# Optimization experiments

Hardware: AMD Instinct MI355X
Metric: run time of the kernel (lower is better)

## Reference

```python
import jax, jax.numpy as jnp
import numpy as np

NPOINT = 1024
BRANCHES = [(0.4, 32), (0.8, 64)]  # (radius, nsample)
SPECS = [[67, 64, 64, 128], [67, 64, 128, 256]]  # mlp specs after use_xyz (+3)
EPS = 1e-5


def setup_inputs() -> dict:
    key = jax.random.key(0)
    ks = jax.random.split(key, 16)
    B, N, C = 8, 8192, 64
    inp = {
        "xyz": jax.random.normal(ks[0], (B, N, 3), jnp.float32),
        "features": jax.random.normal(ks[1], (B, C, N), jnp.float32),
    }
    ki = 2
    for bi, spec in enumerate(SPECS):
        for li in range(3):
            o, i = spec[li + 1], spec[li]
            inp[f"w{bi}_{li}"] = jax.random.normal(ks[ki], (o, i), jnp.float32) * (1.0 / np.sqrt(i)); ki += 1
            inp[f"g{bi}_{li}"] = jnp.ones((o,), jnp.float32)
            inp[f"b{bi}_{li}"] = jnp.zeros((o,), jnp.float32)
    return inp


def fps(pts, npoint):
    # pts: [B, N+1, 3] (mean point prepended); sequential farthest point sampling
    B, N1, _ = pts.shape

    def step(carry, _):
        dist, far = carry
        idx3 = jnp.broadcast_to(far[:, None, None], (B, 1, 3))
        centroid = jnp.take_along_axis(pts, idx3, axis=1)  # [B,1,3]
        d = jnp.sum((pts - centroid) ** 2, axis=-1)        # [B,N+1]
        dist = jnp.minimum(dist, d)
        far2 = jnp.argmax(dist, axis=-1)
        return (dist, far2), centroid[:, 0, :]

    dist0 = jnp.full((B, N1), 1e10, jnp.float32)
    far0 = jnp.zeros((B,), jnp.int32)
    _, locs = jax.lax.scan(step, (dist0, far0), None, length=npoint)
    return jnp.transpose(locs, (1, 0, 2))  # [B, npoint, 3]


def ball_query(xyz, new_xyz, radius, nsample):
    # first <=nsample indices with dist^2 < radius^2, padded with first valid (0 if none)
    B, N, _ = xyz.shape
    d2 = jnp.sum((new_xyz[:, :, None, :] - xyz[:, None, :, :]) ** 2, axis=-1)  # [B,S,N]
    score = jnp.where(d2 < radius * radius, jnp.arange(N, dtype=jnp.int32), N)
    vals, _ = jax.lax.top_k(-score, nsample)  # smallest scores = earliest valid indices
    idx = -vals                               # [B,S,nsample], N marks invalid
    first = idx[..., :1]
    first = jnp.where(first < N, first, 0)
    return jnp.where(idx < N, idx, first)


def _forward(xyz, features, params):
    mean = jnp.mean(xyz, axis=1, keepdims=True)
    pts = jnp.concatenate([mean, xyz], axis=1)          # prepend mean point
    new_xyz = jax.lax.stop_gradient(fps(pts, NPOINT))   # [B,npoint,3] (torch no_grad)
    outs = []
    for (radius, nsample), layers in zip(BRANCHES, params):
        idx = ball_query(xyz, new_xyz, radius, nsample)           # [B,S,K]
        gxyz = jax.vmap(lambda p, i: p[i])(xyz, idx)              # [B,S,K,3]
        rel = jnp.transpose(gxyz - new_xyz[:, :, None, :], (0, 3, 1, 2))  # [B,3,S,K]
        gfeat = jax.vmap(lambda f, i: f[:, i])(features, idx)     # [B,C,S,K]
        x = jnp.concatenate([rel, gfeat], axis=1)                 # [B,3+C,S,K]
        for W, g, b in layers:  # Conv2d 1x1 (no bias) + BatchNorm (train stats) + ReLU
            x = jnp.einsum('oi,bisk->bosk', W, x)
            m = jnp.mean(x, axis=(0, 2, 3), keepdims=True)
            v = jnp.var(x, axis=(0, 2, 3), keepdims=True)
            x = (x - m) / jnp.sqrt(v + EPS) * g[None, :, None, None] + b[None, :, None, None]
            x = jax.nn.relu(x)
        outs.append(jnp.max(x, axis=3))                           # [B,Cout,S]
    return new_xyz, jnp.concatenate(outs, axis=1)


def reference(xyz, features,
              w0_0, g0_0, b0_0, w0_1, g0_1, b0_1, w0_2, g0_2, b0_2,
              w1_0, g1_0, b1_0, w1_1, g1_1, b1_1, w1_2, g1_2, b1_2):
    params = [
        [(w0_0, g0_0, b0_0), (w0_1, g0_1, b0_1), (w0_2, g0_2, b0_2)],
        [(w1_0, g1_0, b1_0), (w1_1, g1_1, b1_1), (w1_2, g1_2, b1_2)],
    ]
    return _forward(xyz, features, params)
```

## Files before the change

### kernel.cpp

```cpp
#include <hip/hip_runtime.h>
#include <hip/hip_bf16.h>
#include <cstdint>


typedef __attribute__((ext_vector_type(8))) short short8;
typedef __attribute__((ext_vector_type(4))) float f32x4;
typedef __attribute__((ext_vector_type(2))) float f32x2;

__device__ __forceinline__ float bf2f(unsigned short u) {
    return __uint_as_float(((unsigned)u) << 16);
}
__device__ __forceinline__ unsigned short f2bf(float f) {
    unsigned u = __float_as_uint(f);
    return (unsigned short)((u + 0x7fffu + ((u >> 16) & 1u)) >> 16);
}

__device__ __forceinline__ float wave_red_max_f32(float v) {
#define DPPSTEP(ctrl)                                                                  \
    {                                                                                  \
        int _t = __builtin_amdgcn_update_dpp((int)0xFF800000, __float_as_int(v), ctrl, \
                                             0xf, 0xf, false);                         \
        v = fmaxf(v, __int_as_float(_t));                                              \
    }
    DPPSTEP(0x111) DPPSTEP(0x112) DPPSTEP(0x114) DPPSTEP(0x118) DPPSTEP(0x142) DPPSTEP(0x143)
#undef DPPSTEP
    return v;
}
__device__ __forceinline__ unsigned wave_red_min_u32(unsigned v) {
#define DPPSTEP(ctrl)                                                                   \
    {                                                                                   \
        unsigned _t = (unsigned)__builtin_amdgcn_update_dpp((int)0xFFFFFFFF, (int)v,    \
                                                            ctrl, 0xf, 0xf, false);     \
        v = v < _t ? v : _t;                                                            \
    }
    DPPSTEP(0x111) DPPSTEP(0x112) DPPSTEP(0x114) DPPSTEP(0x118) DPPSTEP(0x142) DPPSTEP(0x143)
#undef DPPSTEP
    return v;
}
__device__ __forceinline__ unsigned long long u64max(unsigned long long a, unsigned long long b) {
    return a > b ? a : b;
}
__device__ __forceinline__ unsigned u32min(unsigned a, unsigned b) { return a < b ? a : b; }

static const size_t OFF_WBF   = 0;
static const size_t OFF_STATS = 262144;
static const size_t STATS_BYTES = 720896;
static const size_t OFF_AFF   = 1048576;
static const size_t OFF_IDX0  = 2097152;
static const size_t OFF_IDX1  = 3145728;
static const size_t OFF_MX    = 5242880;
static const size_t OFF_MN    = 13631488;
static const size_t OFF_Y0    = 22020096;
static const size_t OFF_Y1    = 90177536;
static const size_t OFF_FEATT = 211812352;

__global__ __launch_bounds__(512) void fused_pre(
    const float* __restrict__ xyz, const float* __restrict__ feat,
    float* __restrict__ newxyz, unsigned short* __restrict__ ft,
    const float* __restrict__ w0, const float* __restrict__ w1, const float* __restrict__ w2,
    const float* __restrict__ w3, const float* __restrict__ w4, const float* __restrict__ w5,
    unsigned short* __restrict__ wb) {
    __shared__ union alignas(16) SM {
        struct {
            float ptsx[8200], ptsy[8200], ptsz[8200];
            float ldsM[16][3];
            float meanv[3];
            unsigned long long sKey[2][8];
            float cbuf[3072];
        } f;
        float tile[64][65];
    } sm;
    const int tid = threadIdx.x;

    if (blockIdx.x >= 1032) {
        int id = (int)(blockIdx.x - 1032) * 512 + tid;
        const int psz[6] = {6144, 4096, 8192, 6144, 8192, 32768};
        const int Kp[6] = {96, 64, 64, 96, 64, 128};
        const int Ks[6] = {67, 64, 64, 67, 64, 128};
        const float* wp[6] = {w0, w1, w2, w3, w4, w5};
        int off = 0;
        for (int l = 0; l < 6; ++l) {
            if (id < off + psz[l]) {
                int e = id - off;
                int m = e / Kp[l], k = e - m * Kp[l];
                float v = (k < Ks[l]) ? wp[l][m * Ks[l] + k] : 0.f;
                wb[id] = f2bf(v);
                return;
            }
            off += psz[l];
        }
        return;
    }

    if (blockIdx.x >= 8) {
        int tb = (int)blockIdx.x - 8;
        int b = tb >> 7;
        int j0 = (tb & 127) * 64;
#pragma unroll
        for (int i = 0; i < 8; ++i) {
            int e = i * 512 + tid;
            int c = e >> 6, j = e & 63;
            sm.tile[j][c] = feat[((size_t)b * 64 + c) * 8192 + j0 + j];
        }
        __syncthreads();
#pragma unroll
        for (int i = 0; i < 8; ++i) {
            int e = i * 512 + tid;
            int j = e >> 6, c = e & 63;
            ft[((size_t)(b * 8192 + j0 + j)) * 96 + 3 + c] = f2bf(sm.tile[j][c]);
        }
        if (tid < 64) {
            int j = tid;
            size_t base = ((size_t)(b * 8192 + j0 + j)) * 96;
            const float* xp = xyz + ((size_t)b * 8192 + j0 + j) * 3;
            ft[base + 0] = f2bf(xp[0]);
            ft[base + 1] = f2bf(xp[1]);
            ft[base + 2] = f2bf(xp[2]);
        } else if (tid < 128) {
            int j = tid - 64;
            size_t base = ((size_t)(b * 8192 + j0 + j)) * 96;
            for (int c = 67; c < 96; ++c) ft[base + c] = 0;
        }
        return;
    }

    const int b = blockIdx.x;
    const int t = tid;
    const int lane = t & 63, wv = t >> 6;
    const float* xb = xyz + (size_t)b * 8192 * 3;

    f32x2 px[8], py[8], pz[8], d[8];
#pragma unroll
    for (int k = 0; k < 8; ++k) {
        int q0 = t + 512 * (2 * k);
        int q1 = t + 512 * (2 * k + 1);
        px[k].x = xb[q0 * 3 + 0]; px[k].y = xb[q1 * 3 + 0];
        py[k].x = xb[q0 * 3 + 1]; py[k].y = xb[q1 * 3 + 1];
        pz[k].x = xb[q0 * 3 + 2]; pz[k].y = xb[q1 * 3 + 2];
        d[k].x = 1e10f; d[k].y = 1e10f;
        sm.f.ptsx[q0 + 1] = px[k].x; sm.f.ptsx[q1 + 1] = px[k].y;
        sm.f.ptsy[q0 + 1] = py[k].x; sm.f.ptsy[q1 + 1] = py[k].y;
        sm.f.ptsz[q0 + 1] = pz[k].x; sm.f.ptsz[q1 + 1] = pz[k].y;
    }
    float sxA = 0.f, syA = 0.f, szA = 0.f;
    float sxB = 0.f, syB = 0.f, szB = 0.f;
    int uA = (t + 1023) & 1023;
    int uB = (t + 511) & 1023;
#pragma unroll
    for (int j = 0; j < 8; ++j) {
        int ia = uA + 1024 * j;
        int ib = uB + 1024 * j;
        sxA += xb[ia * 3 + 0]; syA += xb[ia * 3 + 1]; szA += xb[ia * 3 + 2];
        sxB += xb[ib * 3 + 0]; syB += xb[ib * 3 + 1]; szB += xb[ib * 3 + 2];
    }
#pragma unroll
    for (int off = 32; off; off >>= 1) {
        sxA += __shfl_xor(sxA, off, 64);
        syA += __shfl_xor(syA, off, 64);
        szA += __shfl_xor(szA, off, 64);
        sxB += __shfl_xor(sxB, off, 64);
        syB += __shfl_xor(syB, off, 64);
        szB += __shfl_xor(szB, off, 64);
    }
    if (lane == 0) {
        sm.f.ldsM[wv][0] = sxA; sm.f.ldsM[wv][1] = syA; sm.f.ldsM[wv][2] = szA;
        sm.f.ldsM[wv + 8][0] = sxB; sm.f.ldsM[wv + 8][1] = syB; sm.f.ldsM[wv + 8][2] = szB;
    }
    __syncthreads();
    if (t < 3) {
        float s = 0.f;
        for (int w = 0; w < 16; ++w) s += sm.f.ldsM[w][t];
        sm.f.meanv[t] = s * (1.f / 8192.f);
    }
    __syncthreads();
    float cx = sm.f.meanv[0], cy = sm.f.meanv[1], cz = sm.f.meanv[2];
    const float mmx = cx, mmy = cy, mmz = cz;
    float dm = 1e10f;
    if (t == 0) { sm.f.ptsx[0] = cx; sm.f.ptsy[0] = cy; sm.f.ptsz[0] = cz; }
    __syncthreads();

    for (int it = 0; it < 1024; ++it) {
        if (t == 0) {
            sm.f.cbuf[it * 3 + 0] = cx;
            sm.f.cbuf[it * 3 + 1] = cy;
            sm.f.cbuf[it * 3 + 2] = cz;
        }
        f32x2 c0, c1, c2, vm2;
        c0.x = cx; c0.y = cx; c1.x = cy; c1.y = cy; c2.x = cz; c2.y = cz;
        vm2.x = -1e30f; vm2.y = -1e30f;
        {
#pragma clang fp contract(off)
#pragma unroll
            for (int k = 0; k < 8; ++k) {
                f32x2 dx = px[k] - c0;
                f32x2 dy = py[k] - c1;
                f32x2 dz = pz[k] - c2;
                f32x2 dd = (dx * dx + dy * dy) + dz * dz;
                f32x2 nd = __builtin_elementwise_min(d[k], dd);
                d[k] = nd;
                vm2 = __builtin_elementwise_max(vm2, nd);
            }
        }
        float vmax = fmaxf(vm2.x, vm2.y);
        if (t == 0) {
            float dx = __fsub_rn(mmx, cx);
            float dy = __fsub_rn(mmy, cy);
            float dz = __fsub_rn(mmz, cz);
            float dd = __fadd_rn(__fadd_rn(__fmul_rn(dx, dx), __fmul_rn(dy, dy)), __fmul_rn(dz, dz));
            dm = fminf(dm, dd);
            vmax = fmaxf(vmax, dm);
        }
        float wm = wave_red_max_f32(vmax);
        float bmaxw = __int_as_float(__builtin_amdgcn_readlane(__float_as_int(wm), 63));
        unsigned m2[8];
#pragma unroll
        for (int k = 0; k < 8; ++k) {
            unsigned i0 = (d[k].x == bmaxw) ? (unsigned)(t + 512 * (2 * k) + 1) : 0xFFFFFFFFu;
            unsigned i1 = (d[k].y == bmaxw) ? (unsigned)(t + 512 * (2 * k + 1) + 1) : 0xFFFFFFFFu;
            m2[k] = u32min(i0, i1);
        }
        unsigned n0 = u32min(m2[0], m2[1]), n1 = u32min(m2[2], m2[3]);
        unsigned n2 = u32min(m2[4], m2[5]), n3 = u32min(m2[6], m2[7]);
        unsigned mi = u32min(u32min(n0, n1), u32min(n2, n3));
        if (t == 0 && dm == bmaxw) mi = 0u;
        unsigned wmin = wave_red_min_u32(mi);
        unsigned miw = (unsigned)__builtin_amdgcn_readlane((int)wmin, 63);
        int par = it & 1;
        if (lane == 0)
            sm.f.sKey[par][wv] = ((unsigned long long)__float_as_uint(bmaxw) << 32) |
                                 (unsigned long long)(8192u - miw);
        __syncthreads();
        unsigned long long ka[8];
#pragma unroll
        for (int i = 0; i < 8; ++i) ka[i] = sm.f.sKey[par][i];
        unsigned long long p0 = u64max(ka[0], ka[1]), p1 = u64max(ka[2], ka[3]);
        unsigned long long p2 = u64max(ka[4], ka[5]), p3 = u64max(ka[6], ka[7]);
        unsigned long long kk = u64max(u64max(p0, p1), u64max(p2, p3));
        int far = 8192 - (int)(unsigned)(kk & 0xffffffffull);
        cx = sm.f.ptsx[far];
        cy = sm.f.ptsy[far];
        cz = sm.f.ptsz[far];
    }
    __syncthreads();
    float* ob = newxyz + (size_t)b * 3072;
#pragma unroll
    for (int i = 0; i < 6; ++i) ob[t + 512 * i] = sm.f.cbuf[t + 512 * i];
}

__global__ void ball_query_kernel(const float* __restrict__ xyz, const float* __restrict__ newxyz,
                                  int* __restrict__ idxout, float r2, int K) {
    int wid = (blockIdx.x * blockDim.x + threadIdx.x) >> 6;
    int lane = threadIdx.x & 63;
    int b = wid >> 10;
    const float* q = newxyz + (size_t)wid * 3;
    float qx = q[0], qy = q[1], qz = q[2];
    const float* xb = xyz + (size_t)b * 8192 * 3;
    int* out = idxout + (size_t)wid * K;
    int count = 0;
    int first = 0;
    for (int base = 0; base < 8192 && count < K; base += 64) {
        int j = base + lane;
        float dx = __fsub_rn(xb[j * 3 + 0], qx);
        float dy = __fsub_rn(xb[j * 3 + 1], qy);
        float dz = __fsub_rn(xb[j * 3 + 2], qz);
        float d2 = __fadd_rn(__fadd_rn(__fmul_rn(dx, dx), __fmul_rn(dy, dy)), __fmul_rn(dz, dz));
        bool in = d2 < r2;
        unsigned long long m = __ballot(in);
        if (count == 0 && m) first = base + __ffsll((long long)m) - 1;
        if (in) {
            int pos = count + __popcll(m & ((1ull << lane) - 1ull));
            if (pos < K) out[pos] = j;
        }
        count += __popcll(m);
    }
    if (count < K) {
        int fillv = (count > 0) ? first : 0;
        for (int p = count + lane; p < K; p += 64) out[p] = fillv;
    }
}

template <int Mp, int Kp, int IN_MODE, int OUT_MODE, int KSH>
__global__ __launch_bounds__(256) void gemm_mfma(
    const unsigned short* __restrict__ Wb, const unsigned short* __restrict__ Xin,
    const float* __restrict__ aff, const int* __restrict__ idx,
    const unsigned short* __restrict__ ftp, const float* __restrict__ newxyz,
    unsigned short* __restrict__ Yout, float* __restrict__ MX, float* __restrict__ MN,
    float* __restrict__ statS, float* __restrict__ statQ) {
    constexpr int MT = Mp / 64;
    constexpr int KS = Kp / 32;
    constexpr int Kpad = Kp + 8;
    constexpr int KC = Kp / 8;
    constexpr int CPT = (64 * KC) / 256;
    __shared__ unsigned short Bs[64 * Kpad];
    __shared__ float sAux[256];
    int* sAuxI = (int*)sAux;

    const int tid = threadIdx.x;
    const int w = tid >> 6;
    const int lane = tid & 63;
    const int n = lane & 15;
    const int quad = lane >> 4;
    const int rbase = w * (Mp / 4);
    const long col0 = (long)blockIdx.x * 64;

    short8 a[MT][KS];
#pragma unroll
    for (int mt = 0; mt < MT; ++mt)
#pragma unroll
        for (int ks = 0; ks < KS; ++ks)
            a[mt][ks] = *(const short8*)(Wb + (size_t)(rbase + mt * 16 + n) * Kp + ks * 32 + quad * 8);

    if constexpr (IN_MODE == 0) {
        if (tid < 64) {
            long colg = col0 + tid;
            sAuxI[tid] = idx[colg];
            long sk = colg >> KSH;
            sAux[64 + tid] = newxyz[sk * 3 + 0];
            sAux[128 + tid] = newxyz[sk * 3 + 1];
            sAux[192 + tid] = newxyz[sk * 3 + 2];
        }
    } else {
        if (tid < 2 * Kp) sAux[tid] = aff[tid];
    }
    __syncthreads();

    if constexpr (IN_MODE == 0) {
        const int bb = (int)(col0 >> (KSH + 10));
#pragma unroll
        for (int i = 0; i < CPT; ++i) {
            int c = i * 256 + tid;
            int col = c / KC;
            int kc = c - col * KC;
            int j = sAuxI[col];
            short8 v = *(const short8*)(ftp + ((long)(bb * 8192 + j)) * 96 + kc * 8);
            if (kc == 0) {
                v[0] = (short)f2bf(bf2f((unsigned short)v[0]) - sAux[64 + col]);
                v[1] = (short)f2bf(bf2f((unsigned short)v[1]) - sAux[128 + col]);
                v[2] = (short)f2bf(bf2f((unsigned short)v[2]) - sAux[192 + col]);
            }
            *(short8*)(&Bs[col * Kpad + kc * 8]) = v;
        }
    } else {
#pragma unroll
        for (int i = 0; i < CPT; ++i) {
            int c = i * 256 + tid;
            int col = c / KC;
            int kc = c - col * KC;
            short8 raw = *(const short8*)(Xin + (col0 + col) * (long)Kp + kc * 8);
            short8 v;
#pragma unroll
            for (int e = 0; e < 8; ++e) {
                float xf = bf2f((unsigned short)raw[e]);
                xf = fmaxf(fmaf(xf, sAux[kc * 8 + e], sAux[Kp + kc * 8 + e]), 0.f);
                v[e] = (short)f2bf(xf);
            }
            *(short8*)(&Bs[col * Kpad + kc * 8]) = v;
        }
    }
    __syncthreads();

    f32x4 acc[MT][4];
#pragma unroll
    for (int mt = 0; mt < MT; ++mt)
#pragma unroll
        for (int nt = 0; nt < 4; ++nt)
#pragma unroll
            for (int r = 0; r < 4; ++r) acc[mt][nt][r] = 0.f;

#pragma unroll
    for (int ks = 0; ks < KS; ++ks) {
#pragma unroll
        for (int nt = 0; nt < 4; ++nt) {
            short8 bfr = *(const short8*)(&Bs[(nt * 16 + n) * Kpad + ks * 32 + quad * 8]);
#pragma unroll
            for (int mt = 0; mt < MT; ++mt)
                acc[mt][nt] = __builtin_amdgcn_mfma_f32_16x16x32_bf16(a[mt][ks], bfr, acc[mt][nt], 0, 0, 0);
        }
    }

    const int slot = (int)(blockIdx.x & 127);
#pragma unroll
    for (int mt = 0; mt < MT; ++mt)
#pragma unroll
        for (int r = 0; r < 4; ++r) {
            float s = 0.f, q = 0.f;
#pragma unroll
            for (int nt = 0; nt < 4; ++nt) {
                float v = acc[mt][nt][r];
                s += v;
                q = fmaf(v, v, q);
            }
#pragma unroll
            for (int off = 1; off < 16; off <<= 1) {
                s += __shfl_xor(s, off, 16);
                q += __shfl_xor(q, off, 16);
            }
            if (n == 0) {
                int ch = rbase + mt * 16 + quad * 4 + r;
                atomicAdd(statS + (size_t)ch * 128 + slot, s);
                atomicAdd(statQ + (size_t)ch * 128 + slot, q);
            }
        }

    if constexpr (OUT_MODE == 0) {
#pragma unroll
        for (int mt = 0; mt < MT; ++mt)
#pragma unroll
            for (int nt = 0; nt < 4; ++nt) {
                long col = col0 + nt * 16 + n;
                unsigned p0 = f2bf(acc[mt][nt][0]) | ((unsigned)f2bf(acc[mt][nt][1]) << 16);
                unsigned p1 = f2bf(acc[mt][nt][2]) | ((unsigned)f2bf(acc[mt][nt][3]) << 16);
                uint2 st; st.x = p0; st.y = p1;
                *(uint2*)(Yout + col * Mp + rbase + mt * 16 + quad * 4) = st;
            }
    } else {
#pragma unroll
        for (int mt = 0; mt < MT; ++mt)
#pragma unroll
            for (int r = 0; r < 4; ++r) {
                if constexpr (KSH == 6) {
                    float mx = acc[mt][0][r], mn = acc[mt][0][r];
#pragma unroll
                    for (int nt = 1; nt < 4; ++nt) {
                        mx = fmaxf(mx, acc[mt][nt][r]);
                        mn = fminf(mn, acc[mt][nt][r]);
                    }
#pragma unroll
                    for (int off = 1; off < 16; off <<= 1) {
                        mx = fmaxf(mx, __shfl_xor(mx, off, 16));
                        mn = fminf(mn, __shfl_xor(mn, off, 16));
                    }
                    if (n == 0) {
                        int ch = rbase + mt * 16 + quad * 4 + r;
                        long g = col0 >> 6;
                        MX[(long)ch * 8192 + g] = mx;
                        MN[(long)ch * 8192 + g] = mn;
                    }
                } else {
#pragma unroll
                    for (int gh = 0; gh < 2; ++gh) {
                        float mx = fmaxf(acc[mt][2 * gh][r], acc[mt][2 * gh + 1][r]);
                        float mn = fminf(acc[mt][2 * gh][r], acc[mt][2 * gh + 1][r]);
#pragma unroll
                        for (int off = 1; off < 16; off <<= 1) {
                            mx = fmaxf(mx, __shfl_xor(mx, off, 16));
                            mn = fminf(mn, __shfl_xor(mn, off, 16));
                        }
                        if (n == 0) {
                            int ch = rbase + mt * 16 + quad * 4 + r;
                            long g = (col0 >> 5) + gh;
                            MX[(long)ch * 8192 + g] = mx;
                            MN[(long)ch * 8192 + g] = mn;
                        }
                    }
                }
            }
    }
}

__global__ void finalize_kernel(const float* __restrict__ sS, const float* __restrict__ sQ,
                                const float* __restrict__ g, const float* __restrict__ b,
                                float* __restrict__ aff, int C, float invCount) {
    int c = threadIdx.x + blockIdx.x * blockDim.x;
    if (c >= C) return;
    float s = 0.f, q = 0.f;
    for (int k = 0; k < 128; ++k) { s += sS[c * 128 + k]; q += sQ[c * 128 + k]; }
    float mean = s * invCount;
    float var = fmaxf(q * invCount - mean * mean, 0.f);
    float sc = g[c] / sqrtf(var + 1e-5f);
    float sh = b[c] - mean * sc;
    aff[c] = sc;
    aff[C + c] = sh;
}

__global__ void final_out_kernel(const float* __restrict__ MX, const float* __restrict__ MN,
                                 const float* __restrict__ aff, float* __restrict__ out1,
                                 int Cout, int cOff) {
    long i = (long)blockIdx.x * 256 + threadIdx.x;
    int c = (int)(i >> 13);
    int gidx = (int)(i & 8191);
    int b = gidx >> 10, s = gidx & 1023;
    float sc = aff[c], sh = aff[Cout + c];
    float v = fmaxf(fmaxf(sc * MX[i] + sh, sc * MN[i] + sh), 0.f);
    out1[((long)b * 384 + cOff + c) * 1024 + s] = v;
}

extern "C" void kernel_launch(void* const* d_in, const int* in_sizes, int n_in,
                              void* d_out, int out_size, void* d_ws, size_t ws_size,
                              hipStream_t stream) {
    const float* xyz = (const float*)d_in[0];
    const float* feat = (const float*)d_in[1];
    const float *W[6], *G[6], *Bi[6];
    for (int l = 0; l < 6; ++l) {
        W[l] = (const float*)d_in[2 + l * 3];
        G[l] = (const float*)d_in[3 + l * 3];
        Bi[l] = (const float*)d_in[4 + l * 3];
    }
    char* ws = (char*)d_ws;
    float* out0 = (float*)d_out;
    float* out1 = (float*)d_out + 24576;

    unsigned short* wb = (unsigned short*)(ws + OFF_WBF);
    float* stats = (float*)(ws + OFF_STATS);
    float* affine = (float*)(ws + OFF_AFF);
    int* idx0 = (int*)(ws + OFF_IDX0);
    int* idx1 = (int*)(ws + OFF_IDX1);
    float* mx = (float*)(ws + OFF_MX);
    float* mn = (float*)(ws + OFF_MN);
    unsigned short* y0 = (unsigned short*)(ws + OFF_Y0);
    unsigned short* y1 = (unsigned short*)(ws + OFF_Y1);
    unsigned short* ftp = (unsigned short*)(ws + OFF_FEATT);

    hipMemsetAsync(stats, 0, STATS_BYTES, stream);
    fused_pre<<<1160, 512, 0, stream>>>(xyz, feat, out0, ftp, W[0], W[1], W[2], W[3], W[4],
                                        W[5], wb);

    const int wOff[6] = {0, 6144, 10240, 18432, 24576, 32768};
    int stOff[6], afOff[6];
    {
        const int Cs[6] = {64, 64, 128, 64, 128, 256};
        int so = 0, ao = 0;
        for (int l = 0; l < 6; ++l) {
            stOff[l] = so; so += Cs[l] * 256;
            afOff[l] = ao; ao += Cs[l] * 2;
        }
    }

    for (int br = 0; br < 2; ++br) {
        const int K = br ? 64 : 32;
        const float radius = br ? 0.8f : 0.4f;
        const long NCOL = 8L * 1024 * K;
        int* idx = br ? idx1 : idx0;
        const int l0 = br * 3, l1 = br * 3 + 1, l2 = br * 3 + 2;
        const int M2 = br ? 256 : 128;
        const float invCount = 1.f / (float)NCOL;
        const int nblk = (int)(NCOL / 64);

        ball_query_kernel<<<2048, 256, 0, stream>>>(xyz, out0, idx, radius * radius, K);

        if (br == 0) {
            gemm_mfma<64, 96, 0, 0, 5><<<nblk, 256, 0, stream>>>(
                wb + wOff[l0], nullptr, nullptr, idx, ftp, out0, y0, nullptr, nullptr,
                stats + stOff[l0], stats + stOff[l0] + 64 * 128);
            finalize_kernel<<<1, 256, 0, stream>>>(stats + stOff[l0], stats + stOff[l0] + 64 * 128,
                                                   G[l0], Bi[l0], affine + afOff[l0], 64, invCount);
            gemm_mfma<64, 64, 1, 0, 5><<<nblk, 256, 0, stream>>>(
                wb + wOff[l1], y0, affine + afOff[l0], nullptr, nullptr, nullptr, y1, nullptr,
                nullptr, stats + stOff[l1], stats + stOff[l1] + 64 * 128);
            finalize_kernel<<<1, 256, 0, stream>>>(stats + stOff[l1], stats + stOff[l1] + 64 * 128,
                                                   G[l1], Bi[l1], affine + afOff[l1], 64, invCount);
            gemm_mfma<128, 64, 1, 1, 5><<<nblk, 256, 0, stream>>>(
                wb + wOff[l2], y1, affine + afOff[l1], nullptr, nullptr, nullptr, nullptr, mx, mn,
                stats + stOff[l2], stats + stOff[l2] + 128 * 128);
            finalize_kernel<<<1, 256, 0, stream>>>(stats + stOff[l2], stats + stOff[l2] + 128 * 128,
                                                   G[l2], Bi[l2], affine + afOff[l2], 128, invCount);
        } else {
            gemm_mfma<64, 96, 0, 0, 6><<<nblk, 256, 0, stream>>>(
                wb + wOff[l0], nullptr, nullptr, idx, ftp, out0, y0, nullptr, nullptr,
                stats + stOff[l0], stats + stOff[l0] + 64 * 128);
            finalize_kernel<<<1, 256, 0, stream>>>(stats + stOff[l0], stats + stOff[l0] + 64 * 128,
                                                   G[l0], Bi[l0], affine + afOff[l0], 64, invCount);
            gemm_mfma<128, 64, 1, 0, 6><<<nblk, 256, 0, stream>>>(
                wb + wOff[l1], y0, affine + afOff[l0], nullptr, nullptr, nullptr, y1, nullptr,
                nullptr, stats + stOff[l1], stats + stOff[l1] + 128 * 128);
            finalize_kernel<<<1, 256, 0, stream>>>(stats + stOff[l1], stats + stOff[l1] + 128 * 128,
                                                   G[l1], Bi[l1], affine + afOff[l1], 128, invCount);
            gemm_mfma<256, 128, 1, 1, 6><<<nblk, 256, 0, stream>>>(
                wb + wOff[l2], y1, affine + afOff[l1], nullptr, nullptr, nullptr, nullptr, mx, mn,
                stats + stOff[l2], stats + stOff[l2] + 256 * 128);
            finalize_kernel<<<1, 256, 0, stream>>>(stats + stOff[l2], stats + stOff[l2] + 256 * 128,
                                                   G[l2], Bi[l2], affine + afOff[l2], 256, invCount);
        }

        final_out_kernel<<<(M2 * 8192) / 256, 256, 0, stream>>>(mx, mn, affine + afOff[l2], out1,
                                                                M2, br ? 128 : 0);
    }
}
```

Before: 1.783 ms.

## Fuse BN finalize into GEMMs, merge ball queries, tighten FPS inner loop

The separate single-block finalize kernels are removed. Each GEMM now counts finished blocks with an atomic counter, and the last block computes the BatchNorm scale and shift. The two ball-query launches are merged into one kernel that handles both branches. In the FPS kernel, points are packed as float4 in LDS, the distance math is written as packed-add/mul asm, and the argmax index selection now uses a max-reduction with bound_ctrl DPP moves. These changes aim to cut launch count and serial per-iteration latency in FPS, but they add atomic and fence overhead at the end of every GEMM.

```diff
diff --git a/kernel.cpp b/kernel.cpp
--- a/kernel.cpp
+++ b/kernel.cpp
@@ -15,23 +15,21 @@
     return (unsigned short)((u + 0x7fffu + ((u >> 16) & 1u)) >> 16);
 }
 
-__device__ __forceinline__ float wave_red_max_f32(float v) {
-#define DPPSTEP(ctrl)                                                                  \
-    {                                                                                  \
-        int _t = __builtin_amdgcn_update_dpp((int)0xFF800000, __float_as_int(v), ctrl, \
-                                             0xf, 0xf, false);                         \
-        v = fmaxf(v, __int_as_float(_t));                                              \
+__device__ __forceinline__ float wave_red_max_f32_nn(float v) {
+#define DPPSTEP(ctrl)                                                            \
+    {                                                                            \
+        int _t = __builtin_amdgcn_mov_dpp(__float_as_int(v), ctrl, 0xf, 0xf, true); \
+        v = fmaxf(v, __int_as_float(_t));                                        \
     }
     DPPSTEP(0x111) DPPSTEP(0x112) DPPSTEP(0x114) DPPSTEP(0x118) DPPSTEP(0x142) DPPSTEP(0x143)
 #undef DPPSTEP
     return v;
 }
-__device__ __forceinline__ unsigned wave_red_min_u32(unsigned v) {
-#define DPPSTEP(ctrl)                                                                   \
-    {                                                                                   \
-        unsigned _t = (unsigned)__builtin_amdgcn_update_dpp((int)0xFFFFFFFF, (int)v,    \
-                                                            ctrl, 0xf, 0xf, false);     \
-        v = v < _t ? v : _t;                                                            \
+__device__ __forceinline__ unsigned wave_red_max_u32_nn(unsigned v) {
+#define DPPSTEP(ctrl)                                                              \
+    {                                                                              \
+        unsigned _t = (unsigned)__builtin_amdgcn_mov_dpp((int)v, ctrl, 0xf, 0xf, true); \
+        v = v > _t ? v : _t;                                                       \
     }
     DPPSTEP(0x111) DPPSTEP(0x112) DPPSTEP(0x114) DPPSTEP(0x118) DPPSTEP(0x142) DPPSTEP(0x143)
 #undef DPPSTEP
@@ -40,11 +38,12 @@
 __device__ __forceinline__ unsigned long long u64max(unsigned long long a, unsigned long long b) {
     return a > b ? a : b;
 }
-__device__ __forceinline__ unsigned u32min(unsigned a, unsigned b) { return a < b ? a : b; }
+__device__ __forceinline__ unsigned u32max(unsigned a, unsigned b) { return a > b ? a : b; }
 
 static const size_t OFF_WBF   = 0;
 static const size_t OFF_STATS = 262144;
 static const size_t STATS_BYTES = 720896;
+static const size_t OFF_CTR   = 983040;
 static const size_t OFF_AFF   = 1048576;
 static const size_t OFF_IDX0  = 2097152;
 static const size_t OFF_IDX1  = 3145728;
@@ -62,7 +61,7 @@
     unsigned short* __restrict__ wb) {
     __shared__ union alignas(16) SM {
         struct {
-            float ptsx[8200], ptsy[8200], ptsz[8200];
+            f32x4 ptsP[8200];
             float ldsM[16][3];
             float meanv[3];
             unsigned long long sKey[2][8];
@@ -138,9 +137,16 @@
         py[k].x = xb[q0 * 3 + 1]; py[k].y = xb[q1 * 3 + 1];
         pz[k].x = xb[q0 * 3 + 2]; pz[k].y = xb[q1 * 3 + 2];
         d[k].x = 1e10f; d[k].y = 1e10f;
-        sm.f.ptsx[q0 + 1] = px[k].x; sm.f.ptsx[q1 + 1] = px[k].y;
-        sm.f.ptsy[q0 + 1] = py[k].x; sm.f.ptsy[q1 + 1] = py[k].y;
-        sm.f.ptsz[q0 + 1] = pz[k].x; sm.f.ptsz[q1 + 1] = pz[k].y;
+        f32x4 p0; p0.x = px[k].x; p0.y = py[k].x; p0.z = pz[k].x; p0.w = 0.f;
+        f32x4 p1; p1.x = px[k].y; p1.y = py[k].y; p1.z = pz[k].y; p1.w = 0.f;
+        sm.f.ptsP[q0 + 1] = p0;
+        sm.f.ptsP[q1 + 1] = p1;
+    }
+    unsigned cix[8], ciy[8];
+#pragma unroll
+    for (int k = 0; k < 8; ++k) {
+        cix[k] = 8191u - (unsigned)t - 1024u * k;
+        ciy[k] = cix[k] - 512u;
     }
     float sxA = 0.f, syA = 0.f, szA = 0.f;
     float sxB = 0.f, syB = 0.f, szB = 0.f;
@@ -176,7 +182,10 @@
     float cx = sm.f.meanv[0], cy = sm.f.meanv[1], cz = sm.f.meanv[2];
     const float mmx = cx, mmy = cy, mmz = cz;
     float dm = 1e10f;
-    if (t == 0) { sm.f.ptsx[0] = cx; sm.f.ptsy[0] = cy; sm.f.ptsz[0] = cz; }
+    if (t == 0) {
+        f32x4 pm; pm.x = cx; pm.y = cy; pm.z = cz; pm.w = 0.f;
+        sm.f.ptsP[0] = pm;
+    }
     __syncthreads();
 
     for (int it = 0; it < 1024; ++it) {
@@ -185,23 +194,27 @@
             sm.f.cbuf[it * 3 + 1] = cy;
             sm.f.cbuf[it * 3 + 2] = cz;
         }
-        f32x2 c0, c1, c2, vm2;
-        c0.x = cx; c0.y = cx; c1.x = cy; c1.y = cy; c2.x = cz; c2.y = cz;
-        vm2.x = -1e30f; vm2.y = -1e30f;
-        {
-#pragma clang fp contract(off)
-#pragma unroll
-            for (int k = 0; k < 8; ++k) {
-                f32x2 dx = px[k] - c0;
-                f32x2 dy = py[k] - c1;
-                f32x2 dz = pz[k] - c2;
-                f32x2 dd = (dx * dx + dy * dy) + dz * dz;
-                f32x2 nd = __builtin_elementwise_min(d[k], dd);
-                d[k] = nd;
-                vm2 = __builtin_elementwise_max(vm2, nd);
-            }
-        }
-        float vmax = fmaxf(vm2.x, vm2.y);
+        f32x2 nc0, nc1, nc2;
+        nc0.x = -cx; nc0.y = -cx;
+        nc1.x = -cy; nc1.y = -cy;
+        nc2.x = -cz; nc2.y = -cz;
+        float vmax = 0.f;
+#pragma unroll
+        for (int k = 0; k < 8; ++k) {
+            f32x2 dx, dy, dz, xx, yy, zz, s1, dd;
+            asm("v_pk_add_f32 %0, %1, %2" : "=v"(dx) : "v"(px[k]), "v"(nc0));
+            asm("v_pk_add_f32 %0, %1, %2" : "=v"(dy) : "v"(py[k]), "v"(nc1));
+            asm("v_pk_add_f32 %0, %1, %2" : "=v"(dz) : "v"(pz[k]), "v"(nc2));
+            asm("v_pk_mul_f32 %0, %1, %1" : "=v"(xx) : "v"(dx));
+            asm("v_pk_mul_f32 %0, %1, %1" : "=v"(yy) : "v"(dy));
+            asm("v_pk_mul_f32 %0, %1, %1" : "=v"(zz) : "v"(dz));
+            asm("v_pk_add_f32 %0, %1, %2" : "=v"(s1) : "v"(xx), "v"(yy));
+            asm("v_pk_add_f32 %0, %1, %2" : "=v"(dd) : "v"(s1), "v"(zz));
+            float n0 = fminf(d[k].x, dd.x);
+            float n1 = fminf(d[k].y, dd.y);
+            d[k].x = n0; d[k].y = n1;
+            vmax = fmaxf(vmax, fmaxf(n0, n1));
+        }
         if (t == 0) {
             float dx = __fsub_rn(mmx, cx);
             float dy = __fsub_rn(mmy, cy);
@@ -210,25 +223,21 @@
             dm = fminf(dm, dd);
             vmax = fmaxf(vmax, dm);
         }
-        float wm = wave_red_max_f32(vmax);
+        float wm = wave_red_max_f32_nn(vmax);
         float bmaxw = __int_as_float(__builtin_amdgcn_readlane(__float_as_int(wm), 63));
-        unsigned m2[8];
+        unsigned best = 0u;
 #pragma unroll
         for (int k = 0; k < 8; ++k) {
-            unsigned i0 = (d[k].x == bmaxw) ? (unsigned)(t + 512 * (2 * k) + 1) : 0xFFFFFFFFu;
-            unsigned i1 = (d[k].y == bmaxw) ? (unsigned)(t + 512 * (2 * k + 1) + 1) : 0xFFFFFFFFu;
-            m2[k] = u32min(i0, i1);
-        }
-        unsigned n0 = u32min(m2[0], m2[1]), n1 = u32min(m2[2], m2[3]);
-        unsigned n2 = u32min(m2[4], m2[5]), n3 = u32min(m2[6], m2[7]);
-        unsigned mi = u32min(u32min(n0, n1), u32min(n2, n3));
-        if (t == 0 && dm == bmaxw) mi = 0u;
-        unsigned wmin = wave_red_min_u32(mi);
-        unsigned miw = (unsigned)__builtin_amdgcn_readlane((int)wmin, 63);
+            best = u32max(best, (d[k].x == bmaxw) ? cix[k] : 0u);
+            best = u32max(best, (d[k].y == bmaxw) ? ciy[k] : 0u);
+        }
+        if (t == 0 && dm == bmaxw) best = 8192u;
+        unsigned wbest = wave_red_max_u32_nn(best);
+        unsigned miw = (unsigned)__builtin_amdgcn_readlane((int)wbest, 63);
         int par = it & 1;
         if (lane == 0)
             sm.f.sKey[par][wv] = ((unsigned long long)__float_as_uint(bmaxw) << 32) |
-                                 (unsigned long long)(8192u - miw);
+                                 (unsigned long long)miw;
         __syncthreads();
         unsigned long long ka[8];
 #pragma unroll
@@ -237,9 +246,8 @@
         unsigned long long p2 = u64max(ka[4], ka[5]), p3 = u64max(ka[6], ka[7]);
         unsigned long long kk = u64max(u64max(p0, p1), u64max(p2, p3));
         int far = 8192 - (int)(unsigned)(kk & 0xffffffffull);
-        cx = sm.f.ptsx[far];
-        cy = sm.f.ptsy[far];
-        cz = sm.f.ptsz[far];
+        f32x4 c4 = sm.f.ptsP[far];
+        cx = c4.x; cy = c4.y; cz = c4.z;
     }
     __syncthreads();
     float* ob = newxyz + (size_t)b * 3072;
@@ -247,9 +255,14 @@
     for (int i = 0; i < 6; ++i) ob[t + 512 * i] = sm.f.cbuf[t + 512 * i];
 }
 
-__global__ void ball_query_kernel(const float* __restrict__ xyz, const float* __restrict__ newxyz,
-                                  int* __restrict__ idxout, float r2, int K) {
-    int wid = (blockIdx.x * blockDim.x + threadIdx.x) >> 6;
+__global__ void ball_query2(const float* __restrict__ xyz, const float* __restrict__ newxyz,
+                            int* __restrict__ idx0, int* __restrict__ idx1) {
+    int bid = blockIdx.x;
+    int br = (bid >= 2048);
+    int K = br ? 64 : 32;
+    float r2 = br ? (0.8f * 0.8f) : (0.4f * 0.4f);
+    int* idxout = br ? idx1 : idx0;
+    int wid = (((bid & 2047) * 256) + threadIdx.x) >> 6;
     int lane = threadIdx.x & 63;
     int b = wid >> 10;
     const float* q = newxyz + (size_t)wid * 3;
@@ -285,7 +298,9 @@
     const float* __restrict__ aff, const int* __restrict__ idx,
     const unsigned short* __restrict__ ftp, const float* __restrict__ newxyz,
     unsigned short* __restrict__ Yout, float* __restrict__ MX, float* __restrict__ MN,
-    float* __restrict__ statS, float* __restrict__ statQ) {
+    float* __restrict__ statS, float* __restrict__ statQ,
+    const float* __restrict__ gW, const float* __restrict__ bW, float* __restrict__ affOut,
+    float invCount, int* __restrict__ ctr, int nTot) {
     constexpr int MT = Mp / 64;
     constexpr int KS = Kp / 32;
     constexpr int Kpad = Kp + 8;
@@ -293,6 +308,7 @@
     constexpr int CPT = (64 * KC) / 256;
     __shared__ unsigned short Bs[64 * Kpad];
     __shared__ float sAux[256];
+    __shared__ int lastFlag;
     int* sAuxI = (int*)sAux;
 
     const int tid = threadIdx.x;
@@ -456,21 +472,27 @@
                 }
             }
     }
-}
-
-__global__ void finalize_kernel(const float* __restrict__ sS, const float* __restrict__ sQ,
-                                const float* __restrict__ g, const float* __restrict__ b,
-                                float* __restrict__ aff, int C, float invCount) {
-    int c = threadIdx.x + blockIdx.x * blockDim.x;
-    if (c >= C) return;
-    float s = 0.f, q = 0.f;
-    for (int k = 0; k < 128; ++k) { s += sS[c * 128 + k]; q += sQ[c * 128 + k]; }
-    float mean = s * invCount;
-    float var = fmaxf(q * invCount - mean * mean, 0.f);
-    float sc = g[c] / sqrtf(var + 1e-5f);
-    float sh = b[c] - mean * sc;
-    aff[c] = sc;
-    aff[C + c] = sh;
+
+    __threadfence();
+    if (tid == 0) lastFlag = (atomicAdd(ctr, 1) == nTot - 1) ? 1 : 0;
+    __syncthreads();
+    if (lastFlag) {
+        for (int c = tid; c < Mp; c += 256) {
+            float s = 0.f, q = 0.f;
+            for (int k2 = 0; k2 < 128; ++k2) {
+                s += __hip_atomic_load(&statS[(size_t)c * 128 + k2], __ATOMIC_RELAXED,
+                                       __HIP_MEMORY_SCOPE_AGENT);
+                q += __hip_atomic_load(&statQ[(size_t)c * 128 + k2], __ATOMIC_RELAXED,
+                                       __HIP_MEMORY_SCOPE_AGENT);
+            }
+            float mean = s * invCount;
+            float var = fmaxf(q * invCount - mean * mean, 0.f);
+            float sc = gW[c] / sqrtf(var + 1e-5f);
+            float sh = bW[c] - mean * sc;
+            affOut[c] = sc;
+            affOut[Mp + c] = sh;
+        }
+    }
 }
 
 __global__ void final_out_kernel(const float* __restrict__ MX, const float* __restrict__ MN,
@@ -502,6 +524,7 @@
 
     unsigned short* wb = (unsigned short*)(ws + OFF_WBF);
     float* stats = (float*)(ws + OFF_STATS);
+    int* ctr = (int*)(ws + OFF_CTR);
     float* affine = (float*)(ws + OFF_AFF);
     int* idx0 = (int*)(ws + OFF_IDX0);
     int* idx1 = (int*)(ws + OFF_IDX1);
@@ -511,9 +534,10 @@
     unsigned short* y1 = (unsigned short*)(ws + OFF_Y1);
     unsigned short* ftp = (unsigned short*)(ws + OFF_FEATT);
 
-    hipMemsetAsync(stats, 0, STATS_BYTES, stream);
+    hipMemsetAsync(stats, 0, STATS_BYTES + 64, stream);
     fused_pre<<<1160, 512, 0, stream>>>(xyz, feat, out0, ftp, W[0], W[1], W[2], W[3], W[4],
                                         W[5], wb);
+    ball_query2<<<4096, 256, 0, stream>>>(xyz, out0, idx0, idx1);
 
     const int wOff[6] = {0, 6144, 10240, 18432, 24576, 32768};
     int stOff[6], afOff[6];
@@ -528,7 +552,6 @@
 
     for (int br = 0; br < 2; ++br) {
         const int K = br ? 64 : 32;
-        const float radius = br ? 0.8f : 0.4f;
         const long NCOL = 8L * 1024 * K;
         int* idx = br ? idx1 : idx0;
         const int l0 = br * 3, l1 = br * 3 + 1, l2 = br * 3 + 2;
@@ -536,40 +559,32 @@
         const float invCount = 1.f / (float)NCOL;
         const int nblk = (int)(NCOL / 64);
 
-        ball_query_kernel<<<2048, 256, 0, stream>>>(xyz, out0, idx, radius * radius, K);
-
         if (br == 0) {
             gemm_mfma<64, 96, 0, 0, 5><<<nblk, 256, 0, stream>>>(
                 wb + wOff[l0], nullptr, nullptr, idx, ftp, out0, y0, nullptr, nullptr,
-                stats + stOff[l0], stats + stOff[l0] + 64 * 128);
-            finalize_kernel<<<1, 256, 0, stream>>>(stats + stOff[l0], stats + stOff[l0] + 64 * 128,
-                                                   G[l0], Bi[l0], affine + afOff[l0], 64, invCount);
+                stats + stOff[l0], stats + stOff[l0] + 64 * 128, G[l0], Bi[l0],
+                affine + afOff[l0], invCount, ctr + l0, nblk);
             gemm_mfma<64, 64, 1, 0, 5><<<nblk, 256, 0, stream>>>(
                 wb + wOff[l1], y0, affine + afOff[l0], nullptr, nullptr, nullptr, y1, nullptr,
-                nullptr, stats + stOff[l1], stats + stOff[l1] + 64 * 128);
-            finalize_kernel<<<1, 256, 0, stream>>>(stats + stOff[l1], stats + stOff[l1] + 64 * 128,
-                                                   G[l1], Bi[l1], affine + afOff[l1], 64, invCount);
+                nullptr, stats + stOff[l1], stats + stOff[l1] + 64 * 128, G[l1], Bi[l1],
+                affine + afOff[l1], invCount, ctr + l1, nblk);
             gemm_mfma<128, 64, 1, 1, 5><<<nblk, 256, 0, stream>>>(
                 wb + wOff[l2], y1, affine + afOff[l1], nullptr, nullptr, nullptr, nullptr, mx, mn,
-                stats + stOff[l2], stats + stOff[l2] + 128 * 128);
-            finalize_kernel<<<1, 256, 0, stream>>>(stats + stOff[l2], stats + stOff[l2] + 128 * 128,
-                                                   G[l2], Bi[l2], affine + afOff[l2], 128, invCount);
+                stats + stOff[l2], stats + stOff[l2] + 128 * 128, G[l2], Bi[l2],
+                affine + afOff[l2], invCount, ctr + l2, nblk);
         } else {
             gemm_mfma<64, 96, 0, 0, 6><<<nblk, 256, 0, stream>>>(
                 wb + wOff[l0], nullptr, nullptr, idx, ftp, out0, y0, nullptr, nullptr,
-                stats + stOff[l0], stats + stOff[l0] + 64 * 128);
-            finalize_kernel<<<1, 256, 0, stream>>>(stats + stOff[l0], stats + stOff[l0] + 64 * 128,
-                                                   G[l0], Bi[l0], affine + afOff[l0], 64, invCount);
+                stats + stOff[l0], stats + stOff[l0] + 64 * 128, G[l0], Bi[l0],
+                affine + afOff[l0], invCount, ctr + l0, nblk);
             gemm_mfma<128, 64, 1, 0, 6><<<nblk, 256, 0, stream>>>(
                 wb + wOff[l1], y0, affine + afOff[l0], nullptr, nullptr, nullptr, y1, nullptr,
-                nullptr, stats + stOff[l1], stats + stOff[l1] + 128 * 128);
-            finalize_kernel<<<1, 256, 0, stream>>>(stats + stOff[l1], stats + stOff[l1] + 128 * 128,
-                                                   G[l1], Bi[l1], affine + afOff[l1], 128, invCount);
+                nullptr, stats + stOff[l1], stats + stOff[l1] + 128 * 128, G[l1], Bi[l1],
+                affine + afOff[l1], invCount, ctr + l1, nblk);
             gemm_mfma<256, 128, 1, 1, 6><<<nblk, 256, 0, stream>>>(
                 wb + wOff[l2], y1, affine + afOff[l1], nullptr, nullptr, nullptr, nullptr, mx, mn,
-                stats + stOff[l2], stats + stOff[l2] + 256 * 128);
-            finalize_kernel<<<1, 256, 0, stream>>>(stats + stOff[l2], stats + stOff[l2] + 256 * 128,
-                                                   G[l2], Bi[l2], affine + afOff[l2], 256, invCount);
+                stats + stOff[l2], stats + stOff[l2] + 256 * 128, G[l2], Bi[l2],
+                affine + afOff[l2], invCount, ctr + l2, nblk);
         }
 
         final_out_kernel<<<(M2 * 8192) / 256, 256, 0, stream>>>(mx, mn, affine + afOff[l2], out1,
```

After: 6.595 ms. +269.8%, slower.
